# Kernel tuning notes

Measured on AMD Instinct MI355X. Metric: run time of the kernel, lower is better.

## Reference

```python
import jax, jax.numpy as jnp
import numpy as np

LEAK = 0.01      # torch.nn.LeakyReLU default negative_slope
BN_EPS = 1e-5    # BatchNorm1d default eps
N_NODES, N_EDGES, F_NODE, F_EDGE, HID, N_LAYERS, MID = 100000, 1600000, 64, 16, 64, 3, 128


def _bn(h, g, b):
    # training-mode BatchNorm1d over the node axis (biased variance)
    mu = h.mean(axis=0)
    var = jnp.var(h, axis=0)
    return g * (h - mu) * jax.lax.rsqrt(var + BN_EPS) + b


def _lrelu(h):
    return jnp.where(h >= 0, h, LEAK * h)


def setup_inputs() -> dict:
    key = jax.random.key(0)
    ks = jax.random.split(key, 12)
    s = 0.1  # weight scale
    inp = {}
    inp["x"] = jax.random.normal(ks[0], (N_NODES, F_NODE), jnp.float32)
    inp["edge_index"] = jax.random.randint(ks[1], (2, N_EDGES), 0, N_NODES)
    inp["edge_attr"] = jax.random.normal(ks[2], (N_EDGES, F_EDGE), jnp.float32)
    inp["eps"] = jnp.zeros((N_LAYERS,), jnp.float32)
    inp["We"] = jax.random.normal(ks[3], (N_LAYERS, F_EDGE, HID), jnp.float32) * s
    inp["be"] = jnp.zeros((N_LAYERS, HID), jnp.float32)
    inp["W1"] = jax.random.normal(ks[4], (N_LAYERS, HID, HID), jnp.float32) * s
    inp["b1"] = jnp.zeros((N_LAYERS, HID), jnp.float32)
    inp["g1"] = jnp.ones((N_LAYERS, HID), jnp.float32)
    inp["bt1"] = jnp.zeros((N_LAYERS, HID), jnp.float32)
    inp["W2"] = jax.random.normal(ks[5], (N_LAYERS, HID, HID), jnp.float32) * s
    inp["b2"] = jnp.zeros((N_LAYERS, HID), jnp.float32)
    inp["bn_g"] = jnp.ones((N_LAYERS, HID), jnp.float32)
    inp["bn_b"] = jnp.zeros((N_LAYERS, HID), jnp.float32)
    cat_dim = F_NODE + N_LAYERS * HID  # 256
    inp["Wc1"] = jax.random.normal(ks[6], (cat_dim, MID), jnp.float32) * s
    inp["bc1"] = jnp.zeros((MID,), jnp.float32)
    inp["gc"] = jnp.ones((MID,), jnp.float32)
    inp["btc"] = jnp.zeros((MID,), jnp.float32)
    inp["Wc2"] = jax.random.normal(ks[7], (MID, 1), jnp.float32) * s
    inp["bc2"] = jnp.zeros((1,), jnp.float32)
    return inp


def reference(x, edge_index, edge_attr, eps, We, be, W1, b1, g1, bt1, W2, b2,
              bn_g, bn_b, Wc1, bc1, gc, btc, Wc2, bc2):
    src, dst = edge_index[0], edge_index[1]
    n = x.shape[0]
    xs = [x]
    h = x
    for i in range(N_LAYERS):
        # GINEConv message: relu(x_j + lin_edge(edge_attr)), aggregated by sum at dst
        msg = jax.nn.relu(h[src] + edge_attr @ We[i] + be[i])      # [E, HID]
        agg = jax.ops.segment_sum(msg, dst, num_segments=n)        # [N, HID]
        z = (1.0 + eps[i]) * h + agg
        # GINEConv nn: Linear -> BatchNorm -> LeakyReLU -> Linear
        z = z @ W1[i] + b1[i]
        z = _lrelu(_bn(z, g1[i], bt1[i]))
        z = z @ W2[i] + b2[i]
        # outer BatchNorm + LeakyReLU on all but the last conv layer
        if i != N_LAYERS - 1:
            z = _lrelu(_bn(z, bn_g[i], bn_b[i]))
        xs.append(z)
        h = z
    cat = jnp.concatenate(xs, axis=1)                               # [N, 256]
    o = cat @ Wc1 + bc1
    o = _lrelu(_bn(o, gc, btc))
    o = o @ Wc2 + bc2                                               # [N, 1]
    return o.reshape(-1)                                            # [N]
```

## Files before the change

### kernel.cpp

```cpp
#include <hip/hip_runtime.h>

#define NN   100000
#define NE   1600000
#define FE   16
#define HID  64
#define MID  128
#define CAT  256
#define LEAK 0.01f
#define BNE  1e-5f
#define NT   98

typedef float4 f4;

__device__ __forceinline__ float lrelu(float v){ return v >= 0.f ? v : LEAK * v; }

__global__ void __launch_bounds__(256) k_copy_x(const f4* __restrict__ x4, f4* __restrict__ xs4){
    int idx = blockIdx.x * 256 + threadIdx.x;
    if (idx >= NN * 16) return;
    int n = idx >> 4, j = idx & 15;
    xs4[n * 64 + j] = x4[idx];
}


__global__ void __launch_bounds__(256) k_count(const int* __restrict__ ei, int* __restrict__ deg){
    const int stride = gridDim.x * 256;
    for (int e = blockIdx.x * 256 + threadIdx.x; e < NE; e += stride)
        atomicAdd(&deg[ei[NE + e]], 1);
}

__global__ void __launch_bounds__(256) k_scan1(const int* __restrict__ deg,
        int* __restrict__ roff, int* __restrict__ aux){
    __shared__ int sh[256];
    const int tid = threadIdx.x;
    const int base = blockIdx.x * 1024 + tid * 4;
    int e[4], s = 0;
    #pragma unroll
    for (int j = 0; j < 4; ++j){ int i = base + j; e[j] = (i < NN) ? deg[i] : 0; s += e[j]; }
    sh[tid] = s; __syncthreads();
    for (int off = 1; off < 256; off <<= 1){
        int cur = sh[tid]; int add = (tid >= off) ? sh[tid - off] : 0;
        __syncthreads(); sh[tid] = cur + add; __syncthreads();
    }
    int run = sh[tid] - s;
    #pragma unroll
    for (int j = 0; j < 4; ++j){ int i = base + j; if (i < NN) roff[i] = run; run += e[j]; }
    if (tid == 255) aux[blockIdx.x] = sh[255];
}

__global__ void __launch_bounds__(128) k_scan2(int* __restrict__ aux){
    __shared__ int sh[128];
    const int tid = threadIdx.x;
    int v = (tid < NT) ? aux[tid] : 0;
    sh[tid] = v; __syncthreads();
    for (int off = 1; off < 128; off <<= 1){
        int cur = sh[tid]; int add = (tid >= off) ? sh[tid - off] : 0;
        __syncthreads(); sh[tid] = cur + add; __syncthreads();
    }
    if (tid < NT) aux[tid] = sh[tid] - v;
    if (tid == 0) aux[NT] = sh[127];
}

__global__ void __launch_bounds__(256) k_scan3(int* __restrict__ roff, const int* __restrict__ aux){
    int idx = blockIdx.x * 256 + threadIdx.x;
    if (idx < NN) roff[idx] += aux[idx >> 10];
    if (idx == 0) roff[NN] = aux[NT];
}

__global__ void __launch_bounds__(256) k_scatter(const int* __restrict__ ei,
        const f4* __restrict__ ea4, int* __restrict__ rcur,
        int* __restrict__ ssrc, f4* __restrict__ ea_s){
    const int stride = gridDim.x * 256;
    for (int e = blockIdx.x * 256 + threadIdx.x; e < NE; e += stride){
        int dst = ei[NE + e];
        int pos = atomicAdd(&rcur[dst], 1);
        ssrc[pos] = ei[e];
        f4 a = ea4[e * 4 + 0], b = ea4[e * 4 + 1], c = ea4[e * 4 + 2], d = ea4[e * 4 + 3];
        ea_s[pos * 4 + 0] = a; ea_s[pos * 4 + 1] = b;
        ea_s[pos * 4 + 2] = c; ea_s[pos * 4 + 3] = d;
    }
}

__global__ void __launch_bounds__(256) k_gather(const float* __restrict__ h,
        const int* __restrict__ roff, const int* __restrict__ ssrc,
        const f4* __restrict__ ea_s, const float* __restrict__ We,
        const float* __restrict__ be, float* __restrict__ agg){
    const int lane = threadIdx.x & 63;
    float w[FE];
    #pragma unroll
    for (int k = 0; k < FE; ++k) w[k] = We[k * HID + lane];
    const float bv = be[lane];
    const int nwav = (gridDim.x * 256) >> 6;
    for (int n = (blockIdx.x * 256 + threadIdx.x) >> 6; n < NN; n += nwav){
        int r0 = roff[n], r1 = roff[n + 1];
        float acc = 0.f;
        for (int p = r0; p < r1; ++p){
            int s = ssrc[p];
            float m = bv;
            f4 v0 = ea_s[p * 4 + 0], v1 = ea_s[p * 4 + 1];
            f4 v2 = ea_s[p * 4 + 2], v3 = ea_s[p * 4 + 3];
            m = fmaf(v0.x, w[ 0], m); m = fmaf(v0.y, w[ 1], m); m = fmaf(v0.z, w[ 2], m); m = fmaf(v0.w, w[ 3], m);
            m = fmaf(v1.x, w[ 4], m); m = fmaf(v1.y, w[ 5], m); m = fmaf(v1.z, w[ 6], m); m = fmaf(v1.w, w[ 7], m);
            m = fmaf(v2.x, w[ 8], m); m = fmaf(v2.y, w[ 9], m); m = fmaf(v2.z, w[10], m); m = fmaf(v2.w, w[11], m);
            m = fmaf(v3.x, w[12], m); m = fmaf(v3.y, w[13], m); m = fmaf(v3.z, w[14], m); m = fmaf(v3.w, w[15], m);
            acc += fmaxf(h[(size_t)s * CAT + lane] + m, 0.f);
        }
        agg[n * HID + lane] = acc;
    }
}


__global__ void __launch_bounds__(256) k_mm1(const float* __restrict__ h,
        const float* __restrict__ agg, const float* __restrict__ eps, int li,
        const float* __restrict__ W, const float* __restrict__ b,
        float* __restrict__ z1, float* __restrict__ stats){
    __shared__ float Ws[HID * HID];
    __shared__ float red[2][4][HID];
    for (int j = threadIdx.x; j < HID * HID; j += 256) Ws[j] = W[j];
    __syncthreads();
    const int lane = threadIdx.x & 63;
    const int wib  = threadIdx.x >> 6;
    const int nw   = (gridDim.x * 256) >> 6;
    const float ep1 = 1.f + eps[li];
    const float bv  = b[lane];
    float lsum = 0.f, lsq = 0.f;
    for (int n = (blockIdx.x * 256 + threadIdx.x) >> 6; n < NN; n += nw){
        float inval = fmaf(ep1, h[n * CAT + lane], agg[n * HID + lane]);
        float acc = bv;
        #pragma unroll
        for (int k = 0; k < HID; ++k)
            acc = fmaf(__shfl(inval, k), Ws[k * HID + lane], acc);
        z1[n * HID + lane] = acc;
        lsum += acc; lsq += acc * acc;
    }
    red[0][wib][lane] = lsum; red[1][wib][lane] = lsq;
    __syncthreads();
    if (threadIdx.x < HID){
        float s = 0.f, q = 0.f;
        #pragma unroll
        for (int t = 0; t < 4; ++t){ s += red[0][t][threadIdx.x]; q += red[1][t][threadIdx.x]; }
        atomicAdd(&stats[threadIdx.x], s);
        atomicAdd(&stats[HID + threadIdx.x], q);
    }
}

__global__ void k_finalize(const float* __restrict__ stats, const float* __restrict__ g,
                           const float* __restrict__ bt, float* __restrict__ ac, int width){
    int f = threadIdx.x;
    if (f >= width) return;
    float mean = stats[f] * (1.f / NN);
    float var  = stats[width + f] * (1.f / NN) - mean * mean;
    float a = g[f] * rsqrtf(var + BNE);
    ac[f] = a;
    ac[width + f] = bt[f] - mean * a;
}

template<int STATS>
__global__ void __launch_bounds__(256) k_mm2(const float* __restrict__ z1,
        const float* __restrict__ ac, const float* __restrict__ W,
        const float* __restrict__ b, float* __restrict__ outp, int ostride,
        float* __restrict__ stats){
    __shared__ float Ws[HID * HID];
    __shared__ float red[2][4][HID];
    for (int j = threadIdx.x; j < HID * HID; j += 256) Ws[j] = W[j];
    __syncthreads();
    const int lane = threadIdx.x & 63;
    const int wib  = threadIdx.x >> 6;
    const int nw   = (gridDim.x * 256) >> 6;
    const float a_l = ac[lane], c_l = ac[HID + lane];
    const float bv  = b[lane];
    float lsum = 0.f, lsq = 0.f;
    for (int n = (blockIdx.x * 256 + threadIdx.x) >> 6; n < NN; n += nw){
        float t = lrelu(fmaf(a_l, z1[n * HID + lane], c_l));
        float acc = bv;
        #pragma unroll
        for (int k = 0; k < HID; ++k)
            acc = fmaf(__shfl(t, k), Ws[k * HID + lane], acc);
        outp[n * ostride + lane] = acc;
        if (STATS){ lsum += acc; lsq += acc * acc; }
    }
    if (STATS){
        red[0][wib][lane] = lsum; red[1][wib][lane] = lsq;
        __syncthreads();
        if (threadIdx.x < HID){
            float s = 0.f, q = 0.f;
            #pragma unroll
            for (int t = 0; t < 4; ++t){ s += red[0][t][threadIdx.x]; q += red[1][t][threadIdx.x]; }
            atomicAdd(&stats[threadIdx.x], s);
            atomicAdd(&stats[HID + threadIdx.x], q);
        }
    }
}

__global__ void __launch_bounds__(256) k_apply(const float* __restrict__ z2,
        const float* __restrict__ ac, float* __restrict__ dst){
    int idx = blockIdx.x * 256 + threadIdx.x;
    if (idx >= NN * HID) return;
    int n = idx >> 6, f = idx & 63;
    dst[n * CAT + f] = lrelu(fmaf(ac[f], z2[idx], ac[HID + f]));
}

__global__ void __launch_bounds__(256) k_mmc1(const float* __restrict__ xs,
        const f4* __restrict__ Wc14, const float* __restrict__ bc1,
        float* __restrict__ o1, float* __restrict__ stats){
    __shared__ float ins[32 * CAT];
    __shared__ float Ws[64 * MID];
    const int tid = threadIdx.x;
    const int nb  = blockIdx.x * 32;
    {
        const f4* src = (const f4*)xs + (size_t)nb * (CAT / 4);
        f4* dst = (f4*)ins;
        for (int j = tid; j < 32 * CAT / 4; j += 256) dst[j] = src[j];
    }
    const int fb = (tid & 31) * 4;
    const int ng = tid >> 5;
    float acc[4][4];
    #pragma unroll
    for (int j = 0; j < 4; ++j){ acc[j][0]=0.f; acc[j][1]=0.f; acc[j][2]=0.f; acc[j][3]=0.f; }
    for (int c = 0; c < 4; ++c){
        __syncthreads();
        f4* wd = (f4*)Ws;
        for (int j = tid; j < 2048; j += 256) wd[j] = Wc14[c * 2048 + j];
        __syncthreads();
        const float* i0 = ins + (ng +  0) * CAT + c * 64;
        const float* i1 = ins + (ng +  8) * CAT + c * 64;
        const float* i2 = ins + (ng + 16) * CAT + c * 64;
        const float* i3 = ins + (ng + 24) * CAT + c * 64;
        #pragma unroll 8
        for (int k = 0; k < 64; ++k){
            f4 wv = *(const f4*)&Ws[k * MID + fb];
            float v0 = i0[k], v1 = i1[k], v2 = i2[k], v3 = i3[k];
            acc[0][0]=fmaf(v0,wv.x,acc[0][0]); acc[0][1]=fmaf(v0,wv.y,acc[0][1]); acc[0][2]=fmaf(v0,wv.z,acc[0][2]); acc[0][3]=fmaf(v0,wv.w,acc[0][3]);
            acc[1][0]=fmaf(v1,wv.x,acc[1][0]); acc[1][1]=fmaf(v1,wv.y,acc[1][1]); acc[1][2]=fmaf(v1,wv.z,acc[1][2]); acc[1][3]=fmaf(v1,wv.w,acc[1][3]);
            acc[2][0]=fmaf(v2,wv.x,acc[2][0]); acc[2][1]=fmaf(v2,wv.y,acc[2][1]); acc[2][2]=fmaf(v2,wv.z,acc[2][2]); acc[2][3]=fmaf(v2,wv.w,acc[2][3]);
            acc[3][0]=fmaf(v3,wv.x,acc[3][0]); acc[3][1]=fmaf(v3,wv.y,acc[3][1]); acc[3][2]=fmaf(v3,wv.z,acc[3][2]); acc[3][3]=fmaf(v3,wv.w,acc[3][3]);
        }
    }
    __syncthreads();
    float* reds = ins;
    reds[tid] = 0.f;
    __syncthreads();
    f4 bb = *(const f4*)&bc1[fb];
    float s[4] = {0,0,0,0}, q[4] = {0,0,0,0};
    #pragma unroll
    for (int j = 0; j < 4; ++j){
        int n = nb + ng + 8 * j;
        f4 o;
        o.x = acc[j][0] + bb.x; o.y = acc[j][1] + bb.y;
        o.z = acc[j][2] + bb.z; o.w = acc[j][3] + bb.w;
        *(f4*)&o1[(size_t)n * MID + fb] = o;
        s[0]+=o.x; s[1]+=o.y; s[2]+=o.z; s[3]+=o.w;
        q[0]+=o.x*o.x; q[1]+=o.y*o.y; q[2]+=o.z*o.z; q[3]+=o.w*o.w;
    }
    #pragma unroll
    for (int c2 = 0; c2 < 4; ++c2){
        atomicAdd(&reds[fb + c2], s[c2]);
        atomicAdd(&reds[MID + fb + c2], q[c2]);
    }
    __syncthreads();
    atomicAdd(&stats[tid], reds[tid]);
}

__global__ void __launch_bounds__(256) k_final(const float* __restrict__ o1,
        const float* __restrict__ acC, const float* __restrict__ Wc2,
        const float* __restrict__ bc2, float* __restrict__ out){
    const int lane = threadIdx.x & 63;
    const int nw   = (gridDim.x * 256) >> 6;
    const float a0 = acC[lane],      c0 = acC[MID + lane];
    const float a1 = acC[64 + lane], c1 = acC[MID + 64 + lane];
    const float w0 = Wc2[lane], w1 = Wc2[64 + lane];
    const float bb = bc2[0];
    for (int n = (blockIdx.x * 256 + threadIdx.x) >> 6; n < NN; n += nw){
        float t0 = lrelu(fmaf(a0, o1[(size_t)n * MID + lane], c0));
        float t1 = lrelu(fmaf(a1, o1[(size_t)n * MID + 64 + lane], c1));
        float s = fmaf(t0, w0, t1 * w1);
        #pragma unroll
        for (int m = 32; m > 0; m >>= 1) s += __shfl_xor(s, m);
        if (lane == 0) out[n] = s + bb;
    }
}

extern "C" void kernel_launch(void* const* d_in, const int* in_sizes, int n_in,
                              void* d_out, int out_size, void* d_ws, size_t ws_size,
                              hipStream_t stream){
    (void)in_sizes; (void)n_in; (void)out_size; (void)ws_size;
    const float* x   = (const float*)d_in[0];
    const int*   ei  = (const int*)  d_in[1];
    const float* ea  = (const float*)d_in[2];
    const float* eps = (const float*)d_in[3];
    const float* We  = (const float*)d_in[4];
    const float* be  = (const float*)d_in[5];
    const float* W1  = (const float*)d_in[6];
    const float* b1  = (const float*)d_in[7];
    const float* g1  = (const float*)d_in[8];
    const float* bt1 = (const float*)d_in[9];
    const float* W2  = (const float*)d_in[10];
    const float* b2  = (const float*)d_in[11];
    const float* bng = (const float*)d_in[12];
    const float* bnb = (const float*)d_in[13];
    const float* Wc1 = (const float*)d_in[14];
    const float* bc1 = (const float*)d_in[15];
    const float* gc  = (const float*)d_in[16];
    const float* btc = (const float*)d_in[17];
    const float* Wc2 = (const float*)d_in[18];
    const float* bc2 = (const float*)d_in[19];
    float* out = (float*)d_out;
    float* ws  = (float*)d_ws;

    float* xs    = ws;
    float* agg   = xs  + (size_t)NN * CAT;
    float* z1    = agg + (size_t)NN * HID;
    float* stats = z1  + (size_t)NN * HID;
    float* ac1   = stats + 256;
    float* ac2   = ac1 + 128;
    float* acC   = ac2 + 128;
    int*   roff  = (int*)(acC + 256);
    int*   aux   = roff + 100004;
    int*   rcur  = aux + 128;
    int*   ssrc  = rcur + NN;
    f4*    ea_s  = (f4*)(ssrc + NE);
    float* z2    = agg;
    float* o1    = agg;

    hipMemsetAsync(rcur, 0, NN * sizeof(int), stream);
    k_count  <<<2048, 256, 0, stream>>>(ei, rcur);
    k_scan1  <<<NT,   256, 0, stream>>>(rcur, roff, aux);
    k_scan2  <<<1,    128, 0, stream>>>(aux);
    k_scan3  <<<391,  256, 0, stream>>>(roff, aux);
    hipMemcpyAsync(rcur, roff, NN * sizeof(int), hipMemcpyDeviceToDevice, stream);
    k_scatter<<<2048, 256, 0, stream>>>(ei, (const f4*)ea, rcur, ssrc, ea_s);

    k_copy_x<<<6250, 256, 0, stream>>>((const f4*)x, (f4*)xs);

    for (int i = 0; i < 3; ++i){
        hipMemsetAsync(stats, 0, 256 * sizeof(float), stream);
        k_gather<<<2048, 256, 0, stream>>>(xs + i * HID, roff, ssrc, ea_s,
                                           We + i * FE * HID, be + i * HID, agg);
        k_mm1<<<2048, 256, 0, stream>>>(xs + i * HID, agg, eps, i,
                                        W1 + i * HID * HID, b1 + i * HID, z1, stats);
        k_finalize<<<1, 64, 0, stream>>>(stats, g1 + i * HID, bt1 + i * HID, ac1, HID);
        if (i < 2){
            k_mm2<1><<<2048, 256, 0, stream>>>(z1, ac1, W2 + i * HID * HID, b2 + i * HID,
                                               z2, HID, stats + 128);
            k_finalize<<<1, 64, 0, stream>>>(stats + 128, bng + i * HID, bnb + i * HID, ac2, HID);
            k_apply<<<25000, 256, 0, stream>>>(z2, ac2, xs + (i + 1) * HID);
        } else {
            k_mm2<0><<<2048, 256, 0, stream>>>(z1, ac1, W2 + i * HID * HID, b2 + i * HID,
                                               xs + (i + 1) * HID, CAT, nullptr);
        }
    }

    hipMemsetAsync(stats, 0, 256 * sizeof(float), stream);
    k_mmc1<<<3125, 256, 0, stream>>>(xs, (const f4*)Wc1, bc1, o1, stats);
    k_finalize<<<1, 128, 0, stream>>>(stats, gc, btc, acC, MID);
    k_final<<<6250, 256, 0, stream>>>(o1, acC, Wc2, bc2, out);
}
```

Baseline: 1.760 ms.

## Scatter edge indices instead of edge attributes; gather attributes by original edge id

The CSR build now writes (src, edge_id) int2 pairs in place of a sorted copy of the 16-float edge attributes. This removes a large scatter write of edge attributes. The gather kernel reads the original edge_attr through the edge id, making those reads random rather than sequential across three layers. The gather loop is also unrolled by two to keep more loads in flight, and the node index is made wave-uniform with readfirstlane.

```diff
diff --git a/kernel.cpp b/kernel.cpp
--- a/kernel.cpp
+++ b/kernel.cpp
@@ -67,22 +67,28 @@
 }
 
 __global__ void __launch_bounds__(256) k_scatter(const int* __restrict__ ei,
-        const f4* __restrict__ ea4, int* __restrict__ rcur,
-        int* __restrict__ ssrc, f4* __restrict__ ea_s){
+        int* __restrict__ rcur, int2* __restrict__ pairs){
     const int stride = gridDim.x * 256;
     for (int e = blockIdx.x * 256 + threadIdx.x; e < NE; e += stride){
         int dst = ei[NE + e];
         int pos = atomicAdd(&rcur[dst], 1);
-        ssrc[pos] = ei[e];
-        f4 a = ea4[e * 4 + 0], b = ea4[e * 4 + 1], c = ea4[e * 4 + 2], d = ea4[e * 4 + 3];
-        ea_s[pos * 4 + 0] = a; ea_s[pos * 4 + 1] = b;
-        ea_s[pos * 4 + 2] = c; ea_s[pos * 4 + 3] = d;
-    }
+        pairs[pos] = make_int2(ei[e], e);
+    }
+}
+
+__device__ __forceinline__ float edot(const f4* __restrict__ e, const float* w, float bv){
+    f4 v0 = e[0], v1 = e[1], v2 = e[2], v3 = e[3];
+    float m = bv;
+    m = fmaf(v0.x, w[ 0], m); m = fmaf(v0.y, w[ 1], m); m = fmaf(v0.z, w[ 2], m); m = fmaf(v0.w, w[ 3], m);
+    m = fmaf(v1.x, w[ 4], m); m = fmaf(v1.y, w[ 5], m); m = fmaf(v1.z, w[ 6], m); m = fmaf(v1.w, w[ 7], m);
+    m = fmaf(v2.x, w[ 8], m); m = fmaf(v2.y, w[ 9], m); m = fmaf(v2.z, w[10], m); m = fmaf(v2.w, w[11], m);
+    m = fmaf(v3.x, w[12], m); m = fmaf(v3.y, w[13], m); m = fmaf(v3.z, w[14], m); m = fmaf(v3.w, w[15], m);
+    return m;
 }
 
 __global__ void __launch_bounds__(256) k_gather(const float* __restrict__ h,
-        const int* __restrict__ roff, const int* __restrict__ ssrc,
-        const f4* __restrict__ ea_s, const float* __restrict__ We,
+        const int* __restrict__ roff, const int2* __restrict__ pairs,
+        const f4* __restrict__ ea4, const float* __restrict__ We,
         const float* __restrict__ be, float* __restrict__ agg){
     const int lane = threadIdx.x & 63;
     float w[FE];
@@ -91,20 +97,27 @@
     const float bv = be[lane];
     const int nwav = (gridDim.x * 256) >> 6;
     for (int n = (blockIdx.x * 256 + threadIdx.x) >> 6; n < NN; n += nwav){
-        int r0 = roff[n], r1 = roff[n + 1];
+        const int nu = __builtin_amdgcn_readfirstlane(n);
+        const int r0 = roff[nu], r1 = roff[nu + 1];
         float acc = 0.f;
-        for (int p = r0; p < r1; ++p){
-            int s = ssrc[p];
-            float m = bv;
-            f4 v0 = ea_s[p * 4 + 0], v1 = ea_s[p * 4 + 1];
-            f4 v2 = ea_s[p * 4 + 2], v3 = ea_s[p * 4 + 3];
-            m = fmaf(v0.x, w[ 0], m); m = fmaf(v0.y, w[ 1], m); m = fmaf(v0.z, w[ 2], m); m = fmaf(v0.w, w[ 3], m);
-            m = fmaf(v1.x, w[ 4], m); m = fmaf(v1.y, w[ 5], m); m = fmaf(v1.z, w[ 6], m); m = fmaf(v1.w, w[ 7], m);
-            m = fmaf(v2.x, w[ 8], m); m = fmaf(v2.y, w[ 9], m); m = fmaf(v2.z, w[10], m); m = fmaf(v2.w, w[11], m);
-            m = fmaf(v3.x, w[12], m); m = fmaf(v3.y, w[13], m); m = fmaf(v3.z, w[14], m); m = fmaf(v3.w, w[15], m);
-            acc += fmaxf(h[(size_t)s * CAT + lane] + m, 0.f);
-        }
-        agg[n * HID + lane] = acc;
+        int p = r0;
+        for (; p + 1 < r1; p += 2){
+            int2 pr0 = pairs[p];
+            int2 pr1 = pairs[p + 1];
+            float h0 = h[(size_t)pr0.x * CAT + lane];
+            float h1 = h[(size_t)pr1.x * CAT + lane];
+            float m0 = edot(ea4 + (size_t)pr0.y * 4, w, bv);
+            float m1 = edot(ea4 + (size_t)pr1.y * 4, w, bv);
+            acc += fmaxf(h0 + m0, 0.f);
+            acc += fmaxf(h1 + m1, 0.f);
+        }
+        if (p < r1){
+            int2 pr = pairs[p];
+            float hv = h[(size_t)pr.x * CAT + lane];
+            float m  = edot(ea4 + (size_t)pr.y * 4, w, bv);
+            acc += fmaxf(hv + m, 0.f);
+        }
+        agg[nu * HID + lane] = acc;
     }
 }
 
@@ -316,8 +329,7 @@
     int*   roff  = (int*)(acC + 256);
     int*   aux   = roff + 100004;
     int*   rcur  = aux + 128;
-    int*   ssrc  = rcur + NN;
-    f4*    ea_s  = (f4*)(ssrc + NE);
+    int2*  pairs = (int2*)(rcur + NN);
     float* z2    = agg;
     float* o1    = agg;
 
@@ -327,13 +339,13 @@
     k_scan2  <<<1,    128, 0, stream>>>(aux);
     k_scan3  <<<391,  256, 0, stream>>>(roff, aux);
     hipMemcpyAsync(rcur, roff, NN * sizeof(int), hipMemcpyDeviceToDevice, stream);
-    k_scatter<<<2048, 256, 0, stream>>>(ei, (const f4*)ea, rcur, ssrc, ea_s);
+    k_scatter<<<2048, 256, 0, stream>>>(ei, rcur, pairs);
 
     k_copy_x<<<6250, 256, 0, stream>>>((const f4*)x, (f4*)xs);
 
     for (int i = 0; i < 3; ++i){
         hipMemsetAsync(stats, 0, 256 * sizeof(float), stream);
-        k_gather<<<2048, 256, 0, stream>>>(xs + i * HID, roff, ssrc, ea_s,
+        k_gather<<<2048, 256, 0, stream>>>(xs + i * HID, roff, pairs, (const f4*)ea,
                                            We + i * FE * HID, be + i * HID, agg);
         k_mm1<<<2048, 256, 0, stream>>>(xs + i * HID, agg, eps, i,
                                         W1 + i * HID * HID, b1 + i * HID, z1, stats);
```

After: 1.497 ms. 14.9% less time.
